# Performance work log

Measured on AMD Instinct MI355X. Metric: run time of the kernel, lower is better.

The kernel has to match this reference:

```python
import jax, jax.numpy as jnp
import numpy as np

DIM = 1536      # model dim
NH = 12         # num heads
HD = 128        # head dim
F, H, W = 3, 26, 48   # video latent grid (frames, height, width)
S = F * H * W   # sequence length = 3744
B = 1
EPS = 1e-6
C2 = HD // 2    # 64 rotary pairs per head
SPLITS = [C2 - 2 * (C2 // 3), C2 // 3, C2 // 3]  # [22, 21, 21] for (f, h, w)


def _rope_angles():
    """Wan rope_params: concat of per-axis inverse-frequency angle tables, [1024, 64]."""
    def rp(dim):  # returns [1024, dim//2]
        inv = 1.0 / (10000.0 ** (np.arange(0, dim, 2, dtype=np.float64) / dim))
        return np.outer(np.arange(1024, dtype=np.float64), inv)
    a = np.concatenate([rp(HD - 4 * (HD // 6)), rp(2 * (HD // 6)), rp(2 * (HD // 6))], axis=1)
    return jnp.asarray(a, jnp.float32)


def setup_inputs() -> dict:
    key = jax.random.key(0)
    ks = jax.random.split(key, 9)
    std = DIM ** -0.5
    return {
        "x": jax.random.normal(ks[0], (B, S, DIM), jnp.float32),
        "wq": jax.random.normal(ks[1], (DIM, DIM), jnp.float32) * std,
        "bq": jnp.zeros((DIM,), jnp.float32),
        "wk": jax.random.normal(ks[2], (DIM, DIM), jnp.float32) * std,
        "bk": jnp.zeros((DIM,), jnp.float32),
        "wv": jax.random.normal(ks[3], (DIM, DIM), jnp.float32) * std,
        "bv": jnp.zeros((DIM,), jnp.float32),
        "wo": jax.random.normal(ks[4], (DIM, DIM), jnp.float32) * std,
        "bo": jnp.zeros((DIM,), jnp.float32),
        "gq": jnp.ones((DIM,), jnp.float32),   # WanRMSNorm weight for q
        "gk": jnp.ones((DIM,), jnp.float32),   # WanRMSNorm weight for k
        "freqs": _rope_angles(),                # [1024, 64] rotary angles
        "seq_lens": jnp.full((B,), S, jnp.int32),
    }


def _rmsnorm(y, g):
    return y * jax.lax.rsqrt(jnp.mean(jnp.square(y), axis=-1, keepdims=True) + EPS) * g


def _rope_grid(freqs):
    """Build per-position rotary angles [S, C2] from the 3D grid (F,H,W)."""
    af = freqs[:F, :SPLITS[0]]                       # [F, 22]
    ah = freqs[:H, SPLITS[0]:SPLITS[0] + SPLITS[1]]  # [H, 21]
    aw = freqs[:W, SPLITS[0] + SPLITS[1]:]           # [W, 21]
    ang = jnp.concatenate([
        jnp.broadcast_to(af[:, None, None, :], (F, H, W, SPLITS[0])),
        jnp.broadcast_to(ah[None, :, None, :], (F, H, W, SPLITS[1])),
        jnp.broadcast_to(aw[None, None, :, :], (F, H, W, SPLITS[2])),
    ], axis=-1)
    return ang.reshape(S, C2)


def _rope_apply(t, cos, sin):
    # t: [B, S, NH, HD]; pairs (even, odd) rotated by angle.
    tp = t.reshape(B, S, NH, C2, 2)
    xr, xi = tp[..., 0], tp[..., 1]
    yr = xr * cos - xi * sin
    yi = xr * sin + xi * cos
    return jnp.stack([yr, yi], axis=-1).reshape(B, S, NH, HD)


def reference(x, wq, bq, wk, bk, wv, bv, wo, bo, gq, gk, freqs, seq_lens):
    q = _rmsnorm(x @ wq.T + bq, gq).reshape(B, S, NH, HD)
    k = _rmsnorm(x @ wk.T + bk, gk).reshape(B, S, NH, HD)
    v = (x @ wv.T + bv).reshape(B, S, NH, HD)

    ang = _rope_grid(freqs)                    # [S, C2]
    cos = jnp.cos(ang)[None, :, None, :]       # [1, S, 1, C2]
    sin = jnp.sin(ang)[None, :, None, :]
    q = _rope_apply(q, cos, sin)
    k = _rope_apply(k, cos, sin)

    scale = HD ** -0.5
    scores = jnp.einsum('bqhd,bkhd->bhqk', q, k) * scale   # [B, NH, S, S]
    kmask = jnp.arange(S)[None, :] < seq_lens[:, None]     # [B, S]
    scores = jnp.where(kmask[:, None, None, :], scores, jnp.float32(-1e9))
    attn = jax.nn.softmax(scores, axis=-1)
    out = jnp.einsum('bhqk,bkhd->bqhd', attn, v).reshape(B, S, DIM)
    return out @ wo.T + bo
```

## Files before the change

### kernel.cpp

```cpp
#include <hip/hip_runtime.h>
#include <stdint.h>


#define DIM   1536
#define S_TOT 3744
#define NHEAD 12
#define HD    128
#define QT2   30
#define KVT   59
#define KSPLIT 2

using short8 = __attribute__((ext_vector_type(8))) short;
using f32x4  = __attribute__((ext_vector_type(4))) float;
using f32x16 = __attribute__((ext_vector_type(16))) float;
using f32x2  = __attribute__((ext_vector_type(2))) float;

__device__ __forceinline__ unsigned short f2bf(float f) {
  unsigned u = __builtin_bit_cast(unsigned, f);
  u += 0x7fffu + ((u >> 16) & 1u);
  return (unsigned short)(u >> 16);
}

__device__ __forceinline__ short8 mk8(unsigned a, unsigned b, unsigned c, unsigned d) {
  union { unsigned u[4]; short8 s; } x;
  x.u[0] = a; x.u[1] = b; x.u[2] = c; x.u[3] = d;
  return x.s;
}

__device__ __forceinline__ void gl_lds16(const void* g, void* l) {
  auto gp = (const __attribute__((address_space(1))) unsigned int*)g;
  auto lp = (__attribute__((address_space(3))) unsigned int*)(uintptr_t)l;
  __builtin_amdgcn_global_load_lds(gp, lp, 16, 0, 0);
}

#define NX4 (S_TOT * DIM / 4)
#define NW4 (DIM * DIM / 4)
__global__ __launch_bounds__(256) void cvt5_kernel(
    const float* __restrict__ x, const float* __restrict__ wq,
    const float* __restrict__ wk, const float* __restrict__ wv,
    const float* __restrict__ wo,
    unsigned short* __restrict__ xb, unsigned short* __restrict__ wqb,
    unsigned short* __restrict__ wkb, unsigned short* __restrict__ wvb,
    unsigned short* __restrict__ wob) {
  int gid = blockIdx.x * 256 + threadIdx.x;
  const float* src; unsigned short* dst; int off;
  if (gid < NX4)                { src = x;  dst = xb;  off = gid; }
  else if (gid < NX4 + NW4)     { src = wq; dst = wqb; off = gid - NX4; }
  else if (gid < NX4 + 2 * NW4) { src = wk; dst = wkb; off = gid - NX4 - NW4; }
  else if (gid < NX4 + 3 * NW4) { src = wv; dst = wvb; off = gid - NX4 - 2 * NW4; }
  else if (gid < NX4 + 4 * NW4) { src = wo; dst = wob; off = gid - NX4 - 3 * NW4; }
  else return;
  float4 v = ((const float4*)src)[off];
  ushort4 o;
  o.x = f2bf(v.x); o.y = f2bf(v.y); o.z = f2bf(v.z); o.w = f2bf(v.w);
  ((ushort4*)dst)[off] = o;
}

__device__ __forceinline__ void gemm_body(const unsigned short* __restrict__ A,
                                          const unsigned short* __restrict__ W,
                                          const float* __restrict__ bias,
                                          float* __restrict__ outF,
                                          unsigned short* __restrict__ outB,
                                          int M, int mode) {
  constexpr int K = DIM, N = DIM;
  __shared__ unsigned short As[128 * 32];
  __shared__ unsigned short Ws[128 * 32];
  int tid = threadIdx.x;
  int w = tid >> 6, lane = tid & 63;
  int wr = w >> 1, wc = w & 1, q4 = lane >> 4, ql = lane & 15;
  int m0 = blockIdx.y * 128, n0 = blockIdx.x * 128;

  f32x4 acc[4][4];
  const f32x4 zero4 = {0.f, 0.f, 0.f, 0.f};
#pragma unroll
  for (int i = 0; i < 4; i++)
#pragma unroll
    for (int j = 0; j < 4; j++) acc[i][j] = zero4;

  for (int k0 = 0; k0 < K; k0 += 32) {
    __syncthreads();
#pragma unroll
    for (int r = 0; r < 2; r++) {
      int idx = r * 256 + tid;
      int row = idx >> 2, ch = idx & 3;
      int am = m0 + row; am = (am < M) ? am : (M - 1);
      gl_lds16(A + (size_t)am * K + k0 + ch * 8, &As[idx * 8]);
      gl_lds16(W + (size_t)(n0 + row) * K + k0 + ch * 8, &Ws[idx * 8]);
    }
    __syncthreads();
    short8 af[4], wf[4];
#pragma unroll
    for (int i = 0; i < 4; i++)
      af[i] = *(const short8*)&As[(wr * 64 + i * 16 + ql) * 32 + q4 * 8];
#pragma unroll
    for (int j = 0; j < 4; j++)
      wf[j] = *(const short8*)&Ws[(wc * 64 + j * 16 + ql) * 32 + q4 * 8];
#pragma unroll
    for (int i = 0; i < 4; i++)
#pragma unroll
      for (int j = 0; j < 4; j++)
        acc[i][j] = __builtin_amdgcn_mfma_f32_16x16x32_bf16(af[i], wf[j], acc[i][j], 0, 0, 0);
  }

  float bb[4];
#pragma unroll
  for (int j = 0; j < 4; j++) bb[j] = bias[n0 + wc * 64 + j * 16 + ql];
#pragma unroll
  for (int i = 0; i < 4; i++) {
#pragma unroll
    for (int rg = 0; rg < 4; rg++) {
      int row = m0 + wr * 64 + i * 16 + q4 * 4 + rg;
      if (row < M) {
#pragma unroll
        for (int j = 0; j < 4; j++) {
          int col = n0 + wc * 64 + j * 16 + ql;
          float v = acc[i][j][rg] + bb[j];
          if (mode == 0) outF[(size_t)row * N + col] = v;
          else           outB[(size_t)row * N + col] = f2bf(v);
        }
      }
    }
  }
}

__global__ __launch_bounds__(256) void gemm_qkv_kernel(
    const unsigned short* __restrict__ xb,
    const unsigned short* __restrict__ wqb, const unsigned short* __restrict__ wkb,
    const unsigned short* __restrict__ wvb,
    const float* __restrict__ bq, const float* __restrict__ bk, const float* __restrict__ bv,
    float* __restrict__ Yq, float* __restrict__ Yk, unsigned short* __restrict__ Vb) {
  int z = blockIdx.z;
  const unsigned short* W = (z == 0) ? wqb : ((z == 1) ? wkb : wvb);
  const float* bias       = (z == 0) ? bq  : ((z == 1) ? bk  : bv);
  float* outF             = (z == 0) ? Yq  : Yk;
  gemm_body(xb, W, bias, outF, Vb, S_TOT, (z == 2) ? 1 : 0);
}

__global__ __launch_bounds__(256) void gemm_out_kernel(
    const unsigned short* __restrict__ AO, const unsigned short* __restrict__ wob,
    const float* __restrict__ bo, float* __restrict__ out) {
  gemm_body(AO, wob, bo, out, nullptr, S_TOT, 0);
}

__global__ __launch_bounds__(256) void normrope_kernel(
    const float* __restrict__ Yq, const float* __restrict__ Yk,
    const float* __restrict__ gq, const float* __restrict__ gk,
    const float* __restrict__ freqs,
    unsigned short* __restrict__ Qb, unsigned short* __restrict__ Kb) {
  int s = blockIdx.x;
  int tid = threadIdx.x;
  int w = tid >> 6, lane = tid & 63;
  const f32x2* yq2 = (const f32x2*)(Yq + (size_t)s * DIM);
  const f32x2* yk2 = (const f32x2*)(Yk + (size_t)s * DIM);
  f32x2 vq[3], vk[3];
  float ssq = 0.f, ssk = 0.f;
#pragma unroll
  for (int r = 0; r < 3; r++) {
    int p = tid + 256 * r;
    vq[r] = yq2[p]; vk[r] = yk2[p];
    ssq += vq[r].x * vq[r].x + vq[r].y * vq[r].y;
    ssk += vk[r].x * vk[r].x + vk[r].y * vk[r].y;
  }
#pragma unroll
  for (int d = 1; d < 64; d <<= 1) {
    ssq += __shfl_xor(ssq, d);
    ssk += __shfl_xor(ssk, d);
  }
  __shared__ float rq[4], rk[4];
  if (lane == 0) { rq[w] = ssq; rk[w] = ssk; }
  __syncthreads();
  float tq = rq[0] + rq[1] + rq[2] + rq[3];
  float tk = rk[0] + rk[1] + rk[2] + rk[3];
  const float SM_L2 = 0.08838834764831845f * 1.4426950408889634f;
  float invq = rsqrtf(tq * (1.f / DIM) + 1e-6f) * SM_L2;
  float invk = rsqrtf(tk * (1.f / DIM) + 1e-6f);

  int fi = s / (26 * 48);
  int hi = (s / 48) % 26;
  int wi = s % 48;
#pragma unroll
  for (int r = 0; r < 3; r++) {
    int p = tid + 256 * r;
    int c = p & 63;
    int frow = (c < 22) ? fi : ((c < 43) ? hi : wi);
    float ang = freqs[frow * 64 + c];
    float sn, cs;
    __sincosf(ang, &sn, &cs);
    {
      float a = vq[r].x * invq * gq[2 * p];
      float b = vq[r].y * invq * gq[2 * p + 1];
      ushort2 o; o.x = f2bf(a * cs - b * sn); o.y = f2bf(a * sn + b * cs);
      ((ushort2*)Qb)[(size_t)s * (DIM / 2) + p] = o;
    }
    {
      float a = vk[r].x * invk * gk[2 * p];
      float b = vk[r].y * invk * gk[2 * p + 1];
      ushort2 o; o.x = f2bf(a * cs - b * sn); o.y = f2bf(a * sn + b * cs);
      ((ushort2*)Kb)[(size_t)s * (DIM / 2) + p] = o;
    }
  }
}

__global__ __launch_bounds__(256) void vtrans_kernel(const unsigned short* __restrict__ Vb,
                                                     unsigned short* __restrict__ Vt) {
  int d0 = blockIdx.x * 64, s0 = blockIdx.y * 64;
  __shared__ unsigned short t[64][65];
  int tid = threadIdx.x;
#pragma unroll
  for (int r = 0; r < 4; r++) {
    int idx = r * 256 + tid;
    int sr = idx >> 4, c4 = (idx & 15) * 4;
    ushort4 v; v.x = v.y = v.z = v.w = 0;
    int s = s0 + sr;
    if (s < S_TOT) v = *(const ushort4*)(Vb + (size_t)s * DIM + d0 + c4);
    t[sr][c4 + 0] = v.x; t[sr][c4 + 1] = v.y; t[sr][c4 + 2] = v.z; t[sr][c4 + 3] = v.w;
  }
  __syncthreads();
#pragma unroll
  for (int r = 0; r < 4; r++) {
    int idx = r * 256 + tid;
    int dr = idx >> 4, s4 = (idx & 15) * 4;
    if (s0 + s4 < S_TOT) {
      ushort4 v;
      v.x = t[s4 + 0][dr]; v.y = t[s4 + 1][dr]; v.z = t[s4 + 2][dr]; v.w = t[s4 + 3][dr];
      *(ushort4*)(Vt + (size_t)(d0 + dr) * S_TOT + s0 + s4) = v;
    }
  }
}

__global__ __launch_bounds__(256, 2) void attn_kernel(
    const unsigned short* __restrict__ Qb, const unsigned short* __restrict__ Kb,
    const unsigned short* __restrict__ Vt,
    float* __restrict__ Opart, float2* __restrict__ Ml,
    const int* __restrict__ seq_lens) {
  const int NWG = QT2 * NHEAD * KSPLIT;
  int bid = blockIdx.x;
  int xcd = bid & 7, bix = bid >> 3;
  const int qc = NWG >> 3;
  int wg = xcd * qc + bix;
  int qt  = wg % QT2;
  int rem = wg / QT2;
  int h    = rem >> 1;
  int sidx = rem & 1;
  int tbeg = sidx ? 30 : 0;
  int tend = sidx ? KVT : 30;

  int tid = threadIdx.x;
  int wv = tid >> 6, lane = tid & 63;
  int lo = lane & 31, hf = lane >> 5;
  int seqlen = seq_lens[0]; if (seqlen > S_TOT) seqlen = S_TOT;

  __shared__ unsigned short Kl[2][64 * 128];
  __shared__ unsigned short Vl[2][128 * 64];

  int q0 = qt * 128 + wv * 32;
  bool wact = (q0 < S_TOT);
  const size_t hoff = (size_t)h * HD;

  auto stage = [&](int buf, int t) {
    int k0 = t * 64;
    const unsigned short* kseg = Kb + (size_t)k0 * DIM + hoff;
#pragma unroll
    for (int r = 0; r < 4; r++) {
      int idx = r * 256 + tid;
      int row = idx >> 4, c = idx & 15;
      int g = c ^ (row & 15);
      gl_lds16(kseg + (size_t)row * DIM + g * 8, &Kl[buf][idx * 8]);
    }
    int kmax = S_TOT - 8 - k0;
#pragma unroll
    for (int r = 0; r < 4; r++) {
      int idx = r * 256 + tid;
      int row = idx >> 3, c = idx & 7;
      int g = c ^ (row & 7);
      int kc = g * 8; if (kc > kmax) kc = kmax;
      gl_lds16(Vt + (hoff + row) * S_TOT + k0 + kc, &Vl[buf][idx * 8]);
    }
  };

  short8 qf[8];
  {
    int qrow = q0 + lo; if (qrow > S_TOT - 1) qrow = S_TOT - 1;
#pragma unroll
    for (int ks = 0; ks < 8; ks++)
      qf[ks] = *(const short8*)(Qb + (size_t)qrow * DIM + hoff + ks * 16 + hf * 8);
  }
  asm volatile("s_waitcnt vmcnt(0)" ::: "memory");

  f32x16 o[4];
#pragma unroll
  for (int dq = 0; dq < 4; dq++)
#pragma unroll
    for (int r = 0; r < 16; r++) o[dq][r] = 0.f;
  float m_run = -3.0e38f, l_run = 0.f;

  stage(0, tbeg);

  for (int t = tbeg; t < tend; ++t) {
    int cur = (t - tbeg) & 1;
    int k0 = t * 64;
    __builtin_amdgcn_s_barrier();
    asm volatile("" ::: "memory");
    if (t + 1 < tend) {
      stage(cur ^ 1, t + 1);
      asm volatile("s_waitcnt vmcnt(8)" ::: "memory");
    } else {
      asm volatile("s_waitcnt vmcnt(0)" ::: "memory");
    }
    __builtin_amdgcn_sched_barrier(0);
    __builtin_amdgcn_s_barrier();
    asm volatile("" ::: "memory");
    if (!wact) continue;

    f32x16 s0, s1;
#pragma unroll
    for (int r = 0; r < 16; r++) { s0[r] = 0.f; s1[r] = 0.f; }
    __builtin_amdgcn_s_setprio(1);
#pragma unroll
    for (int ks = 0; ks < 8; ks++) {
      int sl = ((ks * 2 + hf) ^ (lo & 15)) * 8;
      short8 kf0 = *(const short8*)&Kl[cur][lo * 128 + sl];
      short8 kf1 = *(const short8*)&Kl[cur][(32 + lo) * 128 + sl];
      s0 = __builtin_amdgcn_mfma_f32_32x32x16_bf16(kf0, qf[ks], s0, 0, 0, 0);
      s1 = __builtin_amdgcn_mfma_f32_32x32x16_bf16(kf1, qf[ks], s1, 0, 0, 0);
    }
    __builtin_amdgcn_s_setprio(0);

    if (k0 + 64 > seqlen) {
#pragma unroll
      for (int r = 0; r < 16; r++) {
        int key0 = k0 + (r & 3) + 8 * (r >> 2) + 4 * hf;
        if (key0      >= seqlen) s0[r] = -3.0e38f;
        if (key0 + 32 >= seqlen) s1[r] = -3.0e38f;
      }
    }

    float mloc = s0[0];
#pragma unroll
    for (int r = 1; r < 16; r++) mloc = fmaxf(mloc, s0[r]);
#pragma unroll
    for (int r = 0; r < 16; r++) mloc = fmaxf(mloc, s1[r]);
    mloc = fmaxf(mloc, __shfl_xor(mloc, 32));

    if (!__all(mloc <= m_run + 8.0f)) {
      float mnew = fmaxf(m_run, mloc);
      float alpha = exp2f(m_run - mnew);
      m_run = mnew;
      l_run *= alpha;
      int lb = lane & 32;
      float ar[16];
#pragma unroll
      for (int r = 0; r < 16; r++)
        ar[r] = __shfl(alpha, ((r & 3) + 8 * (r >> 2) + 4 * hf) | lb);
#pragma unroll
      for (int dq = 0; dq < 4; dq++)
#pragma unroll
        for (int r = 0; r < 16; r++) o[dq][r] *= ar[r];
    }

    float lloc = 0.f;
    short8 pa[4];
    {
      float p[16];
#pragma unroll
      for (int r = 0; r < 16; r++) { p[r] = exp2f(s0[r] - m_run); lloc += p[r]; }
      unsigned pr[8];
#pragma unroll
      for (int i = 0; i < 8; i++)
        asm("v_cvt_pk_bf16_f32 %0, %1, %2" : "=v"(pr[i]) : "v"(p[2 * i]), "v"(p[2 * i + 1]));
      asm volatile("v_permlane32_swap_b32 %0, %1" : "+v"(pr[0]), "+v"(pr[2]));
      asm volatile("v_permlane32_swap_b32 %0, %1" : "+v"(pr[1]), "+v"(pr[3]));
      asm volatile("v_permlane32_swap_b32 %0, %1" : "+v"(pr[4]), "+v"(pr[6]));
      asm volatile("v_permlane32_swap_b32 %0, %1" : "+v"(pr[5]), "+v"(pr[7]));
      pa[0] = mk8(pr[0], pr[1], pr[2], pr[3]);
      pa[1] = mk8(pr[4], pr[5], pr[6], pr[7]);
    }
    {
      float p[16];
#pragma unroll
      for (int r = 0; r < 16; r++) { p[r] = exp2f(s1[r] - m_run); lloc += p[r]; }
      unsigned pr[8];
#pragma unroll
      for (int i = 0; i < 8; i++)
        asm("v_cvt_pk_bf16_f32 %0, %1, %2" : "=v"(pr[i]) : "v"(p[2 * i]), "v"(p[2 * i + 1]));
      asm volatile("v_permlane32_swap_b32 %0, %1" : "+v"(pr[0]), "+v"(pr[2]));
      asm volatile("v_permlane32_swap_b32 %0, %1" : "+v"(pr[1]), "+v"(pr[3]));
      asm volatile("v_permlane32_swap_b32 %0, %1" : "+v"(pr[4]), "+v"(pr[6]));
      asm volatile("v_permlane32_swap_b32 %0, %1" : "+v"(pr[5]), "+v"(pr[7]));
      pa[2] = mk8(pr[0], pr[1], pr[2], pr[3]);
      pa[3] = mk8(pr[4], pr[5], pr[6], pr[7]);
    }
    lloc += __shfl_xor(lloc, 32);
    l_run += lloc;

    __builtin_amdgcn_s_setprio(1);
#pragma unroll
    for (int kh2 = 0; kh2 < 4; kh2++) {
      int sl = ((kh2 * 2 + hf) ^ (lo & 7)) * 8;
#pragma unroll
      for (int dq = 0; dq < 4; dq++) {
        short8 vb = *(const short8*)&Vl[cur][(dq * 32 + lo) * 64 + sl];
        o[dq] = __builtin_amdgcn_mfma_f32_32x32x16_bf16(pa[kh2], vb, o[dq], 0, 0, 0);
      }
    }
    __builtin_amdgcn_s_setprio(0);
  }

  if (wact) {
    size_t ob = (((size_t)sidx * NHEAD + h) * QT2 + qt) * (128 * 128);
#pragma unroll
    for (int dq = 0; dq < 4; dq++)
#pragma unroll
      for (int r = 0; r < 16; r++) {
        int row = wv * 32 + (r & 3) + 8 * (r >> 2) + 4 * hf;
        Opart[ob + (size_t)row * 128 + dq * 32 + lo] = o[dq][r];
      }
    if (lane < 32) {
      float2 ml; ml.x = m_run; ml.y = l_run;
      Ml[((size_t)(sidx * NHEAD + h) * QT2 + qt) * 128 + wv * 32 + lo] = ml;
    }
  }
}

__global__ __launch_bounds__(256) void reduce_kernel(
    const float* __restrict__ Opart, const float2* __restrict__ Ml,
    unsigned short* __restrict__ AO) {
  int flat = blockIdx.x * 256 + threadIdx.x;
  int d = flat & 127;
  int r = flat >> 7;
  int h = r / S_TOT;
  int q = r - h * S_TOT;
  int qt = q >> 7, qi = q & 127;
  size_t ob = (((size_t)h * QT2) + qt) * (128 * 128) + (size_t)qi * 128 + d;
  const size_t so = (size_t)NHEAD * QT2 * 128 * 128;
  int mb = (h * QT2 + qt) * 128 + qi;
  const int sm = NHEAD * QT2 * 128;
  float2 ml0 = Ml[mb], ml1 = Ml[mb + sm];
  float mm = fmaxf(ml0.x, ml1.x);
  float w0 = exp2f(ml0.x - mm), w1 = exp2f(ml1.x - mm);
  float l = w0 * ml0.y + w1 * ml1.y;
  float v = (w0 * Opart[ob] + w1 * Opart[ob + so]) / l;
  AO[(size_t)q * DIM + h * HD + d] = f2bf(v);
}

extern "C" void kernel_launch(void* const* d_in, const int* in_sizes, int n_in,
                              void* d_out, int out_size, void* d_ws, size_t ws_size,
                              hipStream_t stream) {
  const float* x    = (const float*)d_in[0];
  const float* wq   = (const float*)d_in[1];
  const float* bq   = (const float*)d_in[2];
  const float* wk   = (const float*)d_in[3];
  const float* bk   = (const float*)d_in[4];
  const float* wv   = (const float*)d_in[5];
  const float* bv   = (const float*)d_in[6];
  const float* wo   = (const float*)d_in[7];
  const float* bo   = (const float*)d_in[8];
  const float* gq   = (const float*)d_in[9];
  const float* gk   = (const float*)d_in[10];
  const float* freqs = (const float*)d_in[11];
  const int*   seq  = (const int*)d_in[12];

  char* ws = (char*)d_ws;
  const size_t SZ_X = (size_t)S_TOT * DIM * 2;
  const size_t SZ_W = (size_t)DIM * DIM * 2;
  const size_t SZ_Y = (size_t)S_TOT * DIM * 4;

  size_t off = 0;
  unsigned short* xb  = (unsigned short*)(ws + off); off += SZ_X;
  unsigned short* wob = (unsigned short*)(ws + off); off += SZ_W;
  float*          Yq  = (float*)(ws + off);          off += SZ_Y;
  float*          Yk  = (float*)(ws + off);          off += SZ_Y;
  unsigned short* wqb = (unsigned short*)(ws + off); off += SZ_W;
  unsigned short* wkb = (unsigned short*)(ws + off); off += SZ_W;
  unsigned short* wvb = (unsigned short*)(ws + off); off += SZ_W;
  unsigned short* Vb  = (unsigned short*)(ws + off); off += SZ_X;
  unsigned short* Qb  = (unsigned short*)(ws + off); off += SZ_X;
  unsigned short* Kb  = (unsigned short*)(ws + off); off += SZ_X;
  unsigned short* Vt  = (unsigned short*)(ws + off); off += SZ_X;
  unsigned short* AO  = (unsigned short*)(ws + off); off += SZ_X;

  float*  Opart = (float*)Yq;
  float2* Ml    = (float2*)((char*)Yq +
                  (size_t)KSPLIT * NHEAD * QT2 * 128 * 128 * sizeof(float));

  int total4 = NX4 + 4 * NW4;
  cvt5_kernel<<<dim3((total4 + 255) / 256), 256, 0, stream>>>(
      x, wq, wk, wv, wo, xb, wqb, wkb, wvb, wob);

  gemm_qkv_kernel<<<dim3(DIM / 128, (S_TOT + 127) / 128, 3), 256, 0, stream>>>(
      xb, wqb, wkb, wvb, bq, bk, bv, Yq, Yk, Vb);

  normrope_kernel<<<dim3(S_TOT), 256, 0, stream>>>(Yq, Yk, gq, gk, freqs, Qb, Kb);

  vtrans_kernel<<<dim3(DIM / 64, (S_TOT + 63) / 64), 256, 0, stream>>>(Vb, Vt);

  attn_kernel<<<dim3(QT2 * NHEAD * KSPLIT), 256, 0, stream>>>(
      Qb, Kb, Vt, Opart, Ml, seq);

  reduce_kernel<<<dim3(NHEAD * S_TOT * HD / 256), 256, 0, stream>>>(Opart, Ml, AO);

  gemm_out_kernel<<<dim3(DIM / 128, (S_TOT + 127) / 128), 256, 0, stream>>>(
      AO, wob, bo, (float*)d_out);
}
```

Before: 417.4 us.

## Shrink attention KV tile to 32 keys and split keys three ways

The attention kernel now processes 32-key tiles instead of 64, halving LDS usage per block and raising launch bounds to four blocks per CU. The key range is split into three chunks instead of two, so more workgroups run concurrently, and the reduce kernel now combines three partials. The Ml buffer moves into the xb workspace region to make room for the larger Opart. In exchange, each tile does less MFMA work per barrier and stage, and the reduce pass reads more partial data.

```diff
diff --git a/kernel.cpp b/kernel.cpp
--- a/kernel.cpp
+++ b/kernel.cpp
@@ -7,8 +7,9 @@
 #define NHEAD 12
 #define HD    128
 #define QT2   30
-#define KVT   59
-#define KSPLIT 2
+#define NT32  117
+#define SPL   39
+#define KSPLIT 3
 
 using short8 = __attribute__((ext_vector_type(8))) short;
 using f32x4  = __attribute__((ext_vector_type(4))) float;
@@ -228,7 +229,7 @@
   }
 }
 
-__global__ __launch_bounds__(256, 2) void attn_kernel(
+__global__ __launch_bounds__(256, 4) void attn_kernel(
     const unsigned short* __restrict__ Qb, const unsigned short* __restrict__ Kb,
     const unsigned short* __restrict__ Vt,
     float* __restrict__ Opart, float2* __restrict__ Ml,
@@ -240,28 +241,28 @@
   int wg = xcd * qc + bix;
   int qt  = wg % QT2;
   int rem = wg / QT2;
-  int h    = rem >> 1;
-  int sidx = rem & 1;
-  int tbeg = sidx ? 30 : 0;
-  int tend = sidx ? KVT : 30;
+  int h    = rem / KSPLIT;
+  int sidx = rem % KSPLIT;
+  int tbeg = sidx * SPL;
+  int tend = tbeg + SPL;
 
   int tid = threadIdx.x;
   int wv = tid >> 6, lane = tid & 63;
   int lo = lane & 31, hf = lane >> 5;
   int seqlen = seq_lens[0]; if (seqlen > S_TOT) seqlen = S_TOT;
 
-  __shared__ unsigned short Kl[2][64 * 128];
-  __shared__ unsigned short Vl[2][128 * 64];
+  __shared__ unsigned short Kl[2][32 * 128];
+  __shared__ unsigned short Vl[2][128 * 32];
 
   int q0 = qt * 128 + wv * 32;
   bool wact = (q0 < S_TOT);
   const size_t hoff = (size_t)h * HD;
 
   auto stage = [&](int buf, int t) {
-    int k0 = t * 64;
+    int k0 = t * 32;
     const unsigned short* kseg = Kb + (size_t)k0 * DIM + hoff;
 #pragma unroll
-    for (int r = 0; r < 4; r++) {
+    for (int r = 0; r < 2; r++) {
       int idx = r * 256 + tid;
       int row = idx >> 4, c = idx & 15;
       int g = c ^ (row & 15);
@@ -269,10 +270,10 @@
     }
     int kmax = S_TOT - 8 - k0;
 #pragma unroll
-    for (int r = 0; r < 4; r++) {
+    for (int r = 0; r < 2; r++) {
       int idx = r * 256 + tid;
-      int row = idx >> 3, c = idx & 7;
-      int g = c ^ (row & 7);
+      int row = idx >> 2, c = idx & 3;
+      int g = c ^ (row & 3);
       int kc = g * 8; if (kc > kmax) kc = kmax;
       gl_lds16(Vt + (hoff + row) * S_TOT + k0 + kc, &Vl[buf][idx * 8]);
     }
@@ -298,12 +299,12 @@
 
   for (int t = tbeg; t < tend; ++t) {
     int cur = (t - tbeg) & 1;
-    int k0 = t * 64;
+    int k0 = t * 32;
     __builtin_amdgcn_s_barrier();
     asm volatile("" ::: "memory");
     if (t + 1 < tend) {
       stage(cur ^ 1, t + 1);
-      asm volatile("s_waitcnt vmcnt(8)" ::: "memory");
+      asm volatile("s_waitcnt vmcnt(4)" ::: "memory");
     } else {
       asm volatile("s_waitcnt vmcnt(0)" ::: "memory");
     }
@@ -312,34 +313,31 @@
     asm volatile("" ::: "memory");
     if (!wact) continue;
 
-    f32x16 s0, s1;
-#pragma unroll
-    for (int r = 0; r < 16; r++) { s0[r] = 0.f; s1[r] = 0.f; }
+    f32x16 s0;
+#pragma unroll
+    for (int r = 0; r < 16; r++) s0[r] = 0.f;
     __builtin_amdgcn_s_setprio(1);
 #pragma unroll
     for (int ks = 0; ks < 8; ks++) {
       int sl = ((ks * 2 + hf) ^ (lo & 15)) * 8;
-      short8 kf0 = *(const short8*)&Kl[cur][lo * 128 + sl];
-      short8 kf1 = *(const short8*)&Kl[cur][(32 + lo) * 128 + sl];
-      s0 = __builtin_amdgcn_mfma_f32_32x32x16_bf16(kf0, qf[ks], s0, 0, 0, 0);
-      s1 = __builtin_amdgcn_mfma_f32_32x32x16_bf16(kf1, qf[ks], s1, 0, 0, 0);
+      short8 kf = *(const short8*)&Kl[cur][lo * 128 + sl];
+      s0 = __builtin_amdgcn_mfma_f32_32x32x16_bf16(kf, qf[ks], s0, 0, 0, 0);
     }
     __builtin_amdgcn_s_setprio(0);
 
-    if (k0 + 64 > seqlen) {
+    if (k0 + 32 > seqlen) {
 #pragma unroll
       for (int r = 0; r < 16; r++) {
         int key0 = k0 + (r & 3) + 8 * (r >> 2) + 4 * hf;
-        if (key0      >= seqlen) s0[r] = -3.0e38f;
-        if (key0 + 32 >= seqlen) s1[r] = -3.0e38f;
+        if (key0 >= seqlen) s0[r] = -3.0e38f;
       }
     }
 
-    float mloc = s0[0];
-#pragma unroll
-    for (int r = 1; r < 16; r++) mloc = fmaxf(mloc, s0[r]);
-#pragma unroll
-    for (int r = 0; r < 16; r++) mloc = fmaxf(mloc, s1[r]);
+    float m0a = fmaxf(fmaxf(s0[0], s0[1]), fmaxf(s0[2], s0[3]));
+    float m0b = fmaxf(fmaxf(s0[4], s0[5]), fmaxf(s0[6], s0[7]));
+    float m0c = fmaxf(fmaxf(s0[8], s0[9]), fmaxf(s0[10], s0[11]));
+    float m0d = fmaxf(fmaxf(s0[12], s0[13]), fmaxf(s0[14], s0[15]));
+    float mloc = fmaxf(fmaxf(m0a, m0b), fmaxf(m0c, m0d));
     mloc = fmaxf(mloc, __shfl_xor(mloc, 32));
 
     if (!__all(mloc <= m_run + 8.0f)) {
@@ -359,7 +357,7 @@
     }
 
     float lloc = 0.f;
-    short8 pa[4];
+    short8 pa[2];
     {
       float p[16];
 #pragma unroll
@@ -375,31 +373,16 @@
       pa[0] = mk8(pr[0], pr[1], pr[2], pr[3]);
       pa[1] = mk8(pr[4], pr[5], pr[6], pr[7]);
     }
-    {
-      float p[16];
-#pragma unroll
-      for (int r = 0; r < 16; r++) { p[r] = exp2f(s1[r] - m_run); lloc += p[r]; }
-      unsigned pr[8];
-#pragma unroll
-      for (int i = 0; i < 8; i++)
-        asm("v_cvt_pk_bf16_f32 %0, %1, %2" : "=v"(pr[i]) : "v"(p[2 * i]), "v"(p[2 * i + 1]));
-      asm volatile("v_permlane32_swap_b32 %0, %1" : "+v"(pr[0]), "+v"(pr[2]));
-      asm volatile("v_permlane32_swap_b32 %0, %1" : "+v"(pr[1]), "+v"(pr[3]));
-      asm volatile("v_permlane32_swap_b32 %0, %1" : "+v"(pr[4]), "+v"(pr[6]));
-      asm volatile("v_permlane32_swap_b32 %0, %1" : "+v"(pr[5]), "+v"(pr[7]));
-      pa[2] = mk8(pr[0], pr[1], pr[2], pr[3]);
-      pa[3] = mk8(pr[4], pr[5], pr[6], pr[7]);
-    }
     lloc += __shfl_xor(lloc, 32);
     l_run += lloc;
 
     __builtin_amdgcn_s_setprio(1);
 #pragma unroll
-    for (int kh2 = 0; kh2 < 4; kh2++) {
-      int sl = ((kh2 * 2 + hf) ^ (lo & 7)) * 8;
+    for (int kh2 = 0; kh2 < 2; kh2++) {
+      int sl = ((kh2 * 2 + hf) ^ (lo & 3)) * 8;
 #pragma unroll
       for (int dq = 0; dq < 4; dq++) {
-        short8 vb = *(const short8*)&Vl[cur][(dq * 32 + lo) * 64 + sl];
+        short8 vb = *(const short8*)&Vl[cur][(dq * 32 + lo) * 32 + sl];
         o[dq] = __builtin_amdgcn_mfma_f32_32x32x16_bf16(pa[kh2], vb, o[dq], 0, 0, 0);
       }
     }
@@ -435,11 +418,11 @@
   const size_t so = (size_t)NHEAD * QT2 * 128 * 128;
   int mb = (h * QT2 + qt) * 128 + qi;
   const int sm = NHEAD * QT2 * 128;
-  float2 ml0 = Ml[mb], ml1 = Ml[mb + sm];
-  float mm = fmaxf(ml0.x, ml1.x);
-  float w0 = exp2f(ml0.x - mm), w1 = exp2f(ml1.x - mm);
-  float l = w0 * ml0.y + w1 * ml1.y;
-  float v = (w0 * Opart[ob] + w1 * Opart[ob + so]) / l;
+  float2 ml0 = Ml[mb], ml1 = Ml[mb + sm], ml2 = Ml[mb + 2 * sm];
+  float mm = fmaxf(fmaxf(ml0.x, ml1.x), ml2.x);
+  float w0 = exp2f(ml0.x - mm), w1 = exp2f(ml1.x - mm), w2 = exp2f(ml2.x - mm);
+  float l = w0 * ml0.y + w1 * ml1.y + w2 * ml2.y;
+  float v = (w0 * Opart[ob] + w1 * Opart[ob + so] + w2 * Opart[ob + 2 * so]) / l;
   AO[(size_t)q * DIM + h * HD + d] = f2bf(v);
 }
 
@@ -480,8 +463,7 @@
   unsigned short* AO  = (unsigned short*)(ws + off); off += SZ_X;
 
   float*  Opart = (float*)Yq;
-  float2* Ml    = (float2*)((char*)Yq +
-                  (size_t)KSPLIT * NHEAD * QT2 * 128 * 128 * sizeof(float));
+  float2* Ml    = (float2*)xb;
 
   int total4 = NX4 + 4 * NW4;
   cvt5_kernel<<<dim3((total4 + 255) / 256), 256, 0, stream>>>(
```

Measured after the change: 584.0 us. 1.4x slower.
